# Kernel tuning notes

Hardware: AMD Instinct MI355X
Metric: run time of the kernel (lower is better)

## Reference

```python
import jax, jax.numpy as jnp
import numpy as np
jax.config.update("jax_enable_x64", True)


def setup_inputs() -> dict:
    key = jax.random.key(0)
    k0, k1, k2 = jax.random.split(key, 3)
    B, T, D, H, NX = 4, 4096, 1024, 32, 12
    NV = D // H  # 32
    x = jax.random.normal(k0, (B, T, D), jnp.float32)
    wx = jax.random.normal(k1, (D, H * NX), jnp.float32) / np.sqrt(D).astype(np.float32)
    wv = jax.random.normal(k2, (D, H * NV), jnp.float32) / np.sqrt(D).astype(np.float32)
    emb0 = jnp.full((D,), -1e-5, jnp.float32)
    emb1 = jnp.full((D,), +1e-5, jnp.float32)
    return {"x": x, "wx": wx, "wv": wv, "emb0": emb0, "emb1": emb1,
            "num_x_bits": NX, "num_v_bits": NV}


def _pack_bits(logits, B, T, H, nb):
    # (logits > 0) -> [B,T,H,nb] -> [B,H,T,nb] -> packed int64 keys [B,H,T]
    bits = (logits > 0).reshape(B, T, H, nb).transpose(0, 2, 1, 3).astype(jnp.int64)
    r = jnp.arange(nb, dtype=jnp.int64)
    return jnp.sum(bits << r, axis=-1)


def _rosa_scan(keys, vals, num_x_bits):
    # Sequential associative-memory automaton, vectorized over (B, H) streams.
    # State: table[b,h,key] (2^num_x_bits slots, init 0).
    # Per step t: y_t = table[key_t] (read), then table[key_t] = v_t (write).
    B, H, T = keys.shape
    table0 = jnp.zeros((B, H, 1 << num_x_bits), jnp.int64)
    bi = jnp.arange(B)[:, None]
    hi = jnp.arange(H)[None, :]

    def step(table, kv):
        k, v = kv  # [B,H]
        y = table[bi, hi, k]
        return table.at[bi, hi, k].set(v), y

    _, ys = jax.lax.scan(step, table0,
                         (keys.transpose(2, 0, 1), vals.transpose(2, 0, 1)))
    return ys.transpose(1, 2, 0)  # [B,H,T]


def reference(x, wx, wv, emb0, emb1, num_x_bits, num_v_bits):
    B, T, D = x.shape
    H = D // num_v_bits
    xx = x @ wx  # [B,T,H*nx]
    xv = x @ wv  # [B,T,H*nv]
    kx = _pack_bits(xx, B, T, H, num_x_bits)  # [B,H,T] int keys
    kv = _pack_bits(xv, B, T, H, num_v_bits)  # [B,H,T] int values
    y = _rosa_scan(kx, kv, num_x_bits)        # [B,H,T] recalled values
    rv = jnp.arange(num_v_bits, dtype=jnp.int64)
    m = ((y[..., None] >> rv) & 1).astype(bool)      # [B,H,T,nv]
    m = m.transpose(0, 2, 1, 3).reshape(B, T, D)      # [B,T,D]
    return jnp.where(m, emb1, emb0)
```

## Files before the change

kernel.cpp:

```cpp
#include <hip/hip_runtime.h>
#include <stdint.h>

#define B_ 4
#define T_ 4096
#define D_ 1024
#define H_ 32
#define NX_ 12
#define NV_ 32
#define NCOL 1408
#define TAU 2e-4f
#define BITW 88

typedef __attribute__((ext_vector_type(8))) short short8v;
typedef __attribute__((ext_vector_type(4))) float floatx4;

static __device__ __forceinline__ unsigned short bf16_rne(float f) {
  unsigned u = __float_as_uint(f);
  return (unsigned short)((u + 0x7FFFu + ((u >> 16) & 1u)) >> 16);
}
static __device__ __forceinline__ float bf16_to_f32(unsigned short h) {
  return __uint_as_float(((unsigned)h) << 16);
}


__global__ __launch_bounds__(256) void wsplit_kernel(
    const float* __restrict__ wx, const float* __restrict__ wv,
    unsigned short* __restrict__ WT)
{
  __shared__ float tile[64][65];
  const int tid = threadIdx.x;
  const int cb = blockIdx.x % (NCOL / 64);
  const int kb = blockIdx.x / (NCOL / 64);
  const int c_local = tid & 63;
  const int c_glob = cb * 64 + c_local;

#pragma unroll
  for (int i = 0; i < 16; ++i) {
    const int k_local = (tid >> 6) + i * 4;
    const int k_glob = kb * 64 + k_local;
    const float v = (c_glob < 384) ? wx[k_glob * 384 + c_glob]
                                   : wv[k_glob * 1024 + (c_glob - 384)];
    tile[k_local][c_local] = v;
  }
  __syncthreads();

#pragma unroll
  for (int i = 0; i < 4; ++i) {
    const int q = (tid >> 6) * 4 + i;
    const int k0 = q * 4;
    const int ks32 = kb * 2 + (k0 >> 5);
    const int kr = k0 & 31;
    const int half = kr >> 4;
    const int g = (kr & 15) >> 2;
    const int lane = g * 16 + (c_glob & 15);
    const int ct = c_glob >> 4;
    const long base = ((long)ks32 * 88 + ct) * 1024 + lane * 8 + half * 4;
    ushort4 hv, lv;
    float f0 = tile[k0 + 0][c_local], f1 = tile[k0 + 1][c_local];
    float f2 = tile[k0 + 2][c_local], f3 = tile[k0 + 3][c_local];
    hv.x = bf16_rne(f0); lv.x = bf16_rne(f0 - bf16_to_f32(hv.x));
    hv.y = bf16_rne(f1); lv.y = bf16_rne(f1 - bf16_to_f32(hv.y));
    hv.z = bf16_rne(f2); lv.z = bf16_rne(f2 - bf16_to_f32(hv.z));
    hv.w = bf16_rne(f3); lv.w = bf16_rne(f3 - bf16_to_f32(hv.w));
    *(ushort4*)&WT[base] = hv;
    *(ushort4*)&WT[base + 512] = lv;
  }
}

__global__ __launch_bounds__(256) void xsplit_kernel(
    const float* __restrict__ x,
    unsigned short* __restrict__ XTh, unsigned short* __restrict__ XTl)
{
  const long q = (long)blockIdx.x * 256 + threadIdx.x;
  const int row = (int)(q >> 8);
  const int k0 = ((int)q & 255) * 4;
  const float4 f = *(const float4*)(x + (long)row * 1024 + k0);
  const int rt = row >> 4, r15 = row & 15;
  const int ks = k0 >> 5, kr = k0 & 31;
  const int half = kr >> 4;
  const int g = (kr & 15) >> 2;
  const int lane = g * 16 + r15;
  const long base = ((long)ks * 1024 + rt) * 512 + lane * 8 + half * 4;
  ushort4 hv, lv;
  hv.x = bf16_rne(f.x); lv.x = bf16_rne(f.x - bf16_to_f32(hv.x));
  hv.y = bf16_rne(f.y); lv.y = bf16_rne(f.y - bf16_to_f32(hv.y));
  hv.z = bf16_rne(f.z); lv.z = bf16_rne(f.z - bf16_to_f32(hv.z));
  hv.w = bf16_rne(f.w); lv.w = bf16_rne(f.w - bf16_to_f32(hv.w));
  *(ushort4*)&XTh[base] = hv;
  *(ushort4*)&XTl[base] = lv;
}

__global__ __launch_bounds__(256, 2) void gemm_kernel(
    const float* __restrict__ x,
    const unsigned short* __restrict__ XTh,
    const unsigned short* __restrict__ XTl,
    const unsigned short* __restrict__ WT,
    const float* __restrict__ wx, const float* __restrict__ wv,
    unsigned short* __restrict__ bitmat)
{
  const int tid = threadIdx.x;
  const int wid = tid >> 6, lane = tid & 63;
  const int wr = wid >> 1, wc = wid & 1;
  const int sw = (blockIdx.x & 7) * 176 + (blockIdx.x >> 3);
  const int bx = sw % 11;
  const int by = sw / 11;

  const int rt0 = by * 8 + wr * 4;
  const int ct0 = bx * 8 + wc * 4;
  const int l8 = lane * 8;

  floatx4 acc[4][4];
#pragma unroll
  for (int i = 0; i < 4; ++i)
#pragma unroll
    for (int j = 0; j < 4; ++j) acc[i][j] = (floatx4)0.f;

  short8v ah0[4], al0[4], bh0[4], bl0[4];
  short8v ah1[4], al1[4], bh1[4], bl1[4];

#define LOADSET(AH, AL, BH, BL, KS)                                           \
  {                                                                           \
    _Pragma("unroll")                                                         \
    for (int mi = 0; mi < 4; ++mi) {                                          \
      const long abase = ((long)(KS) * 1024 + rt0 + mi) * 512 + l8;           \
      AH[mi] = *(const short8v*)&XTh[abase];                                  \
      AL[mi] = *(const short8v*)&XTl[abase];                                  \
    }                                                                         \
    _Pragma("unroll")                                                         \
    for (int nj = 0; nj < 4; ++nj) {                                          \
      const long wbase = ((long)(KS) * 88 + ct0 + nj) * 1024 + l8;            \
      BH[nj] = *(const short8v*)&WT[wbase];                                   \
      BL[nj] = *(const short8v*)&WT[wbase + 512];                             \
    }                                                                         \
  }

#define MFMASET(AH, AL, BH, BL)                                               \
  {                                                                           \
    _Pragma("unroll")                                                         \
    for (int mi = 0; mi < 4; ++mi)                                            \
      _Pragma("unroll")                                                       \
      for (int nj = 0; nj < 4; ++nj) {                                        \
        acc[mi][nj] = __builtin_amdgcn_mfma_f32_16x16x32_bf16(                \
            AH[mi], BH[nj], acc[mi][nj], 0, 0, 0);                            \
        acc[mi][nj] = __builtin_amdgcn_mfma_f32_16x16x32_bf16(                \
            AH[mi], BL[nj], acc[mi][nj], 0, 0, 0);                            \
        acc[mi][nj] = __builtin_amdgcn_mfma_f32_16x16x32_bf16(                \
            AL[mi], BH[nj], acc[mi][nj], 0, 0, 0);                            \
      }                                                                       \
  }

  LOADSET(ah0, al0, bh0, bl0, 0)
#pragma unroll 1
  for (int t = 0; t < 16; ++t) {
    LOADSET(ah1, al1, bh1, bl1, 2 * t + 1)
    __builtin_amdgcn_sched_barrier(0);
    MFMASET(ah0, al0, bh0, bl0)
    if (t < 15) { LOADSET(ah0, al0, bh0, bl0, 2 * t + 2) }
    __builtin_amdgcn_sched_barrier(0);
    MFMASET(ah1, al1, bh1, bl1)
  }

#pragma unroll
  for (int mi = 0; mi < 4; ++mi)
#pragma unroll
    for (int nj = 0; nj < 4; ++nj) {
      const int colg = bx * 128 + wc * 64 + nj * 16 + (lane & 15);
      const int rowbase = by * 128 + wr * 64 + mi * 16 + ((lane >> 4) * 4);
      const int col16 = bx * 8 + wc * 4 + nj;
#pragma unroll
      for (int r = 0; r < 4; ++r) {
        const float v = acc[mi][nj][r];
        bool pos = v > 0.f;
        if (fabsf(v) < TAU) {
          const float* xr = x + (long)(rowbase + r) * 1024;
          const float* wp; int ldw;
          if (colg < 384) { wp = wx + colg; ldw = 384; }
          else            { wp = wv + (colg - 384); ldw = 1024; }
          double s0 = 0, s1 = 0, s2 = 0, s3 = 0;
          for (int d = 0; d < 1024; d += 4) {
            s0 = fma((double)xr[d + 0], (double)wp[(long)(d + 0) * ldw], s0);
            s1 = fma((double)xr[d + 1], (double)wp[(long)(d + 1) * ldw], s1);
            s2 = fma((double)xr[d + 2], (double)wp[(long)(d + 2) * ldw], s2);
            s3 = fma((double)xr[d + 3], (double)wp[(long)(d + 3) * ldw], s3);
          }
          pos = ((s0 + s1) + (s2 + s3)) > 0.0;
        }
        const unsigned long long mask = __ballot(pos);
        if ((lane & 15) == 0)
          bitmat[(long)(rowbase + r) * BITW + col16] =
              (unsigned short)((mask >> (lane & 48)) & 0xFFFFull);
      }
    }
}

__global__ __launch_bounds__(256, 2) void gemm_fb_kernel(
    const float* __restrict__ x,
    const unsigned short* __restrict__ WT,
    const float* __restrict__ wx, const float* __restrict__ wv,
    unsigned short* __restrict__ bitmat)
{
  const int tid = threadIdx.x;
  const int wid = tid >> 6, lane = tid & 63;
  const int wr = wid >> 1, wc = wid & 1;
  const int sw = (blockIdx.x & 7) * 176 + (blockIdx.x >> 3);
  const int bx = sw % 11;
  const int by = sw / 11;

  const int ln15 = lane & 15, g = lane >> 4;
  const int g4 = g * 4;
  const int ct0 = bx * 8 + wc * 4;
  const float* xA = x + (size_t)(by * 128 + wr * 64 + ln15) * 1024;

  floatx4 acc[4][4];
#pragma unroll
  for (int i = 0; i < 4; ++i)
#pragma unroll
    for (int j = 0; j < 4; ++j) acc[i][j] = (floatx4)0.f;

#pragma unroll 1
  for (int ks = 0; ks < 32; ++ks) {
    float4 Aa[4], Ab[4];
    short8v bh[4], bl[4];
#pragma unroll
    for (int mi = 0; mi < 4; ++mi) {
      const float* xp = xA + (size_t)mi * 16384 + ks * 32 + g4;
      Aa[mi] = *(const float4*)xp;
      Ab[mi] = *(const float4*)(xp + 16);
    }
#pragma unroll
    for (int nj = 0; nj < 4; ++nj) {
      const unsigned short* wp =
          WT + ((size_t)ks * 88 + ct0 + nj) * 1024 + lane * 8;
      bh[nj] = *(const short8v*)wp;
      bl[nj] = *(const short8v*)(wp + 512);
    }
    short8v ah[4], al[4];
#pragma unroll
    for (int mi = 0; mi < 4; ++mi) {
      const float fe[8] = {Aa[mi].x, Aa[mi].y, Aa[mi].z, Aa[mi].w,
                           Ab[mi].x, Ab[mi].y, Ab[mi].z, Ab[mi].w};
#pragma unroll
      for (int e = 0; e < 8; ++e) {
        const unsigned short hh = bf16_rne(fe[e]);
        ah[mi][e] = (short)hh;
        al[mi][e] = (short)bf16_rne(fe[e] - bf16_to_f32(hh));
      }
    }
#pragma unroll
    for (int mi = 0; mi < 4; ++mi)
#pragma unroll
      for (int nj = 0; nj < 4; ++nj) {
        acc[mi][nj] = __builtin_amdgcn_mfma_f32_16x16x32_bf16(
            ah[mi], bh[nj], acc[mi][nj], 0, 0, 0);
        acc[mi][nj] = __builtin_amdgcn_mfma_f32_16x16x32_bf16(
            ah[mi], bl[nj], acc[mi][nj], 0, 0, 0);
        acc[mi][nj] = __builtin_amdgcn_mfma_f32_16x16x32_bf16(
            al[mi], bh[nj], acc[mi][nj], 0, 0, 0);
      }
  }

#pragma unroll
  for (int mi = 0; mi < 4; ++mi)
#pragma unroll
    for (int nj = 0; nj < 4; ++nj) {
      const int colg = bx * 128 + wc * 64 + nj * 16 + (lane & 15);
      const int rowbase = by * 128 + wr * 64 + mi * 16 + ((lane >> 4) * 4);
      const int col16 = bx * 8 + wc * 4 + nj;
#pragma unroll
      for (int r = 0; r < 4; ++r) {
        const float v = acc[mi][nj][r];
        bool pos = v > 0.f;
        if (fabsf(v) < TAU) {
          const float* xr = x + (long)(rowbase + r) * 1024;
          const float* wp; int ldw;
          if (colg < 384) { wp = wx + colg; ldw = 384; }
          else            { wp = wv + (colg - 384); ldw = 1024; }
          double s0 = 0, s1 = 0, s2 = 0, s3 = 0;
          for (int d = 0; d < 1024; d += 4) {
            s0 = fma((double)xr[d + 0], (double)wp[(long)(d + 0) * ldw], s0);
            s1 = fma((double)xr[d + 1], (double)wp[(long)(d + 1) * ldw], s1);
            s2 = fma((double)xr[d + 2], (double)wp[(long)(d + 2) * ldw], s2);
            s3 = fma((double)xr[d + 3], (double)wp[(long)(d + 3) * ldw], s3);
          }
          pos = ((s0 + s1) + (s2 + s3)) > 0.0;
        }
        const unsigned long long mask = __ballot(pos);
        if ((lane & 15) == 0)
          bitmat[(long)(rowbase + r) * BITW + col16] =
              (unsigned short)((mask >> (lane & 48)) & 0xFFFFull);
      }
    }
}

__global__ __launch_bounds__(256) void pack_kernel(
    const unsigned short* __restrict__ bitmat,
    unsigned short* __restrict__ kxg, unsigned int* __restrict__ kvg)
{
  const int gid = blockIdx.x * 256 + threadIdx.x;
  const int row = gid >> 5;
  const int h = gid & 31;
  const int b = row >> 12, t = row & (T_ - 1);
  const unsigned short* bp = bitmat + (long)row * BITW;
  const int bitpos = h * NX_;
  const int w0 = bitpos >> 4, off = bitpos & 15;
  const unsigned int v32 = (unsigned int)bp[w0] | ((unsigned int)bp[w0 + 1] << 16);
  const unsigned int key = (v32 >> off) & 0xFFFu;
  const unsigned int val = (unsigned int)bp[24 + 2 * h] |
                           ((unsigned int)bp[25 + 2 * h] << 16);
  const long sidx = ((long)b * H_ + h) * T_ + t;
  kxg[sidx] = (unsigned short)key;
  kvg[sidx] = val;
}

#define CH 1024
#define UNR 16

__global__ __launch_bounds__(256) void scan_kernel(
    const unsigned short* __restrict__ kxg,
    const unsigned int* __restrict__ kvg,
    unsigned int* __restrict__ yg)
{
  __shared__ unsigned int table[1 << NX_];
  __shared__ unsigned int kbuf[CH], vbuf[CH], ybuf[CH];
  const int tid = threadIdx.x;
  const long base = (long)blockIdx.x * T_;

#pragma unroll
  for (int i = 0; i < (1 << NX_) / 256; ++i) table[tid + 256 * i] = 0u;

  for (int c = 0; c < T_ / CH; ++c) {
    __syncthreads();
#pragma unroll
    for (int i = 0; i < CH / 256; ++i) {
      kbuf[tid + 256 * i] = kxg[base + c * CH + tid + 256 * i];
      vbuf[tid + 256 * i] = kvg[base + c * CH + tid + 256 * i];
    }
    __syncthreads();
    if (tid == 0) {
      for (int i = 0; i < CH; i += UNR) {
        unsigned int k[UNR], v[UNR], y[UNR];
#pragma unroll
        for (int u = 0; u < UNR; ++u) { k[u] = kbuf[i + u]; v[u] = vbuf[i + u]; }
#pragma unroll
        for (int u = 0; u < UNR; ++u) { y[u] = table[k[u]]; table[k[u]] = v[u]; }
#pragma unroll
        for (int u = 0; u < UNR; ++u) ybuf[i + u] = y[u];
      }
    }
    __syncthreads();
#pragma unroll
    for (int i = 0; i < CH / 256; ++i)
      yg[base + c * CH + tid + 256 * i] = ybuf[tid + 256 * i];
  }
}

__global__ __launch_bounds__(256) void out_kernel(
    const unsigned int* __restrict__ yg,
    const float* __restrict__ e0, const float* __restrict__ e1,
    float* __restrict__ out)
{
  const int tid = threadIdx.x;
  const int bt = blockIdx.x;
  const int b = bt >> 12, t = bt & (T_ - 1);
  const int h = tid >> 3;
  const unsigned int y = yg[((long)b * H_ + h) * T_ + t];
  const int d0 = tid * 4;
  const int vsh = (tid & 7) * 4;
  float4 o;
  o.x = ((y >> (vsh + 0)) & 1) ? e1[d0 + 0] : e0[d0 + 0];
  o.y = ((y >> (vsh + 1)) & 1) ? e1[d0 + 1] : e0[d0 + 1];
  o.z = ((y >> (vsh + 2)) & 1) ? e1[d0 + 2] : e0[d0 + 2];
  o.w = ((y >> (vsh + 3)) & 1) ? e1[d0 + 3] : e0[d0 + 3];
  *(float4*)&out[(long)bt * D_ + d0] = o;
}

extern "C" void kernel_launch(void* const* d_in, const int* in_sizes, int n_in,
                              void* d_out, int out_size, void* d_ws, size_t ws_size,
                              hipStream_t stream)
{
  const float* x  = (const float*)d_in[0];
  const float* wx = (const float*)d_in[1];
  const float* wv = (const float*)d_in[2];
  const float* e0 = (const float*)d_in[3];
  const float* e1 = (const float*)d_in[4];

  char* ws = (char*)d_ws;
  const size_t MB = 1u << 20;
  unsigned short* WT     = (unsigned short*)(ws + 0 * MB);
  unsigned short* bitmat = (unsigned short*)(ws + 6 * MB);
  unsigned short* kxg    = (unsigned short*)(ws + 9 * MB);
  unsigned int*   kvg    = (unsigned int*)  (ws + 10 * MB);
  unsigned int*   yg     = (unsigned int*)  (ws + 12 * MB);
  unsigned short* XTh    = (unsigned short*)(ws + 14 * MB);
  unsigned short* XTl    = (unsigned short*)(ws + 46 * MB);
  float* out = (float*)d_out;

  const bool fast = ws_size >= (size_t)78 * MB;

  hipLaunchKernelGGL(wsplit_kernel, dim3((NCOL / 64) * 16), dim3(256), 0, stream,
                     wx, wv, WT);
  if (fast) {
    hipLaunchKernelGGL(xsplit_kernel, dim3(16384), dim3(256), 0, stream,
                       x, XTh, XTl);
    hipLaunchKernelGGL(gemm_kernel, dim3(11 * 128), dim3(256), 0, stream,
                       x, XTh, XTl, WT, wx, wv, bitmat);
  } else {
    hipLaunchKernelGGL(gemm_fb_kernel, dim3(11 * 128), dim3(256), 0, stream,
                       x, WT, wx, wv, bitmat);
  }
  hipLaunchKernelGGL(pack_kernel, dim3(2048), dim3(256), 0, stream,
                     bitmat, kxg, kvg);
  hipLaunchKernelGGL(scan_kernel, dim3(B_ * H_), dim3(256), 0, stream,
                     kxg, kvg, yg);
  hipLaunchKernelGGL(out_kernel, dim3(B_ * T_), dim3(256), 0, stream,
                     yg, e0, e1, out);
}
```

Measured before the change: 828.7 us.

## Stage GEMM B tiles in LDS via global_load_lds with double buffering

The GEMM kernel's weight (B) operand is now staged cooperatively into a double-buffered shared-memory tile using direct global-to-LDS loads. Each wave then reads its B fragments from LDS instead of loading them separately from global memory. This removes the duplicate B loads across the two wave rows that use the same columns. It adds two block barriers per iteration and drops the explicit sched_barrier software pipelining, so waits on outstanding A loads at each barrier may reduce overlap.

```diff
diff --git a/kernel.cpp b/kernel.cpp
--- a/kernel.cpp
+++ b/kernel.cpp
@@ -98,6 +98,8 @@
     const float* __restrict__ wx, const float* __restrict__ wv,
     unsigned short* __restrict__ bitmat)
 {
+  __shared__ unsigned short Blds[2][8192];
+
   const int tid = threadIdx.x;
   const int wid = tid >> 6, lane = tid & 63;
   const int wr = wid >> 1, wc = wid & 1;
@@ -106,7 +108,6 @@
   const int by = sw / 11;
 
   const int rt0 = by * 8 + wr * 4;
-  const int ct0 = bx * 8 + wc * 4;
   const int l8 = lane * 8;
 
   floatx4 acc[4][4];
@@ -115,10 +116,22 @@
 #pragma unroll
     for (int j = 0; j < 4; ++j) acc[i][j] = (floatx4)0.f;
 
-  short8v ah0[4], al0[4], bh0[4], bl0[4];
-  short8v ah1[4], al1[4], bh1[4], bl1[4];
-
-#define LOADSET(AH, AL, BH, BL, KS)                                           \
+  short8v ah0[4], al0[4], ah1[4], al1[4];
+
+#define STAGE_B(BUF, KS)                                                      \
+  {                                                                           \
+    const unsigned short* wsrc = WT + ((size_t)(KS) * 88 + bx * 8) * 1024;    \
+    _Pragma("unroll")                                                         \
+    for (int i = 0; i < 4; ++i) {                                             \
+      const int off = (i * 256 + tid) * 8;                                    \
+      __builtin_amdgcn_global_load_lds(                                       \
+          (const __attribute__((address_space(1))) unsigned int*)(wsrc + off),\
+          (__attribute__((address_space(3))) unsigned int*)&Blds[BUF][off],   \
+          16, 0, 0);                                                          \
+    }                                                                         \
+  }
+
+#define LOAD_A(AH, AL, KS)                                                    \
   {                                                                           \
     _Pragma("unroll")                                                         \
     for (int mi = 0; mi < 4; ++mi) {                                          \
@@ -126,38 +139,45 @@
       AH[mi] = *(const short8v*)&XTh[abase];                                  \
       AL[mi] = *(const short8v*)&XTl[abase];                                  \
     }                                                                         \
+  }
+
+#define COMPUTE(AH, AL, BUF)                                                  \
+  {                                                                           \
+    short8v bh[4], bl[4];                                                     \
     _Pragma("unroll")                                                         \
     for (int nj = 0; nj < 4; ++nj) {                                          \
-      const long wbase = ((long)(KS) * 88 + ct0 + nj) * 1024 + l8;            \
-      BH[nj] = *(const short8v*)&WT[wbase];                                   \
-      BL[nj] = *(const short8v*)&WT[wbase + 512];                             \
+      const int boff = (wc * 4 + nj) * 1024 + l8;                             \
+      bh[nj] = *(const short8v*)&Blds[BUF][boff];                             \
+      bl[nj] = *(const short8v*)&Blds[BUF][boff + 512];                       \
     }                                                                         \
-  }
-
-#define MFMASET(AH, AL, BH, BL)                                               \
-  {                                                                           \
     _Pragma("unroll")                                                         \
     for (int mi = 0; mi < 4; ++mi)                                            \
       _Pragma("unroll")                                                       \
       for (int nj = 0; nj < 4; ++nj) {                                        \
         acc[mi][nj] = __builtin_amdgcn_mfma_f32_16x16x32_bf16(                \
-            AH[mi], BH[nj], acc[mi][nj], 0, 0, 0);                            \
+            AH[mi], bh[nj], acc[mi][nj], 0, 0, 0);                            \
         acc[mi][nj] = __builtin_amdgcn_mfma_f32_16x16x32_bf16(                \
-            AH[mi], BL[nj], acc[mi][nj], 0, 0, 0);                            \
+            AH[mi], bl[nj], acc[mi][nj], 0, 0, 0);                            \
         acc[mi][nj] = __builtin_amdgcn_mfma_f32_16x16x32_bf16(                \
-            AL[mi], BH[nj], acc[mi][nj], 0, 0, 0);                            \
+            AL[mi], bh[nj], acc[mi][nj], 0, 0, 0);                            \
       }                                                                       \
   }
 
-  LOADSET(ah0, al0, bh0, bl0, 0)
+  STAGE_B(0, 0)
+  LOAD_A(ah0, al0, 0)
+
 #pragma unroll 1
   for (int t = 0; t < 16; ++t) {
-    LOADSET(ah1, al1, bh1, bl1, 2 * t + 1)
-    __builtin_amdgcn_sched_barrier(0);
-    MFMASET(ah0, al0, bh0, bl0)
-    if (t < 15) { LOADSET(ah0, al0, bh0, bl0, 2 * t + 2) }
-    __builtin_amdgcn_sched_barrier(0);
-    MFMASET(ah1, al1, bh1, bl1)
+    __syncthreads();
+    STAGE_B(1, 2 * t + 1)
+    LOAD_A(ah1, al1, 2 * t + 1)
+    COMPUTE(ah0, al0, 0)
+    __syncthreads();
+    if (t < 15) {
+      STAGE_B(0, 2 * t + 2)
+      LOAD_A(ah0, al0, 2 * t + 2)
+    }
+    COMPUTE(ah1, al1, 1)
   }
 
 #pragma unroll
@@ -402,10 +422,10 @@
   if (fast) {
     hipLaunchKernelGGL(xsplit_kernel, dim3(16384), dim3(256), 0, stream,
                        x, XTh, XTl);
-    hipLaunchKernelGGL(gemm_kernel, dim3(11 * 128), dim3(256), 0, stream,
+    hipLaunchKernelGGL(gemm_kernel, dim3(128 * 11), dim3(256), 0, stream,
                        x, XTh, XTl, WT, wx, wv, bitmat);
   } else {
-    hipLaunchKernelGGL(gemm_fb_kernel, dim3(11 * 128), dim3(256), 0, stream,
+    hipLaunchKernelGGL(gemm_fb_kernel, dim3(128 * 11), dim3(256), 0, stream,
                        x, WT, wx, wv, bitmat);
   }
   hipLaunchKernelGGL(pack_kernel, dim3(2048), dim3(256), 0, stream,
```

Result: no change. 838.2 us (+1.1%).
